# Optimization experiments

Hardware: AMD Instinct MI355X
Metric: run time of the kernel (lower is better)

Reference implementation:

```python
import jax, jax.numpy as jnp
import numpy as np
import math

EMBED_DIM = 2048
NUM_HEADS = 16
HEAD_DIM = EMBED_DIM // NUM_HEADS
SCALE = 1.0 / math.sqrt(HEAD_DIM)

# ALiBi slopes for power-of-2 num_heads: base = 2**(-2**(-(log2(H)-3))), slopes = base**i, i=1..H
_BASE = 2.0 ** (-2.0 ** (-(math.log2(NUM_HEADS) - 3)))
ALIBI_SLOPES = np.array([_BASE ** i for i in range(1, NUM_HEADS + 1)], dtype=np.float32)


def setup_inputs() -> dict:
    key = jax.random.key(0)
    ks = jax.random.split(key, 7)
    B, L, D, R_KV, R_Q = 2, 2048, EMBED_DIM, 512, 1536
    std = 0.02
    return {
        "hidden_states": jax.random.normal(ks[0], (B, L, D), jnp.float32),
        "Wq_down": jax.random.normal(ks[1], (R_Q, D), jnp.float32) * std,
        "Wq_up": jax.random.normal(ks[2], (NUM_HEADS * HEAD_DIM, R_Q), jnp.float32) * std,
        "Wkv_down": jax.random.normal(ks[3], (R_KV, D), jnp.float32) * std,
        "k_up": jax.random.normal(ks[4], (NUM_HEADS, R_KV, HEAD_DIM), jnp.float32) * std,
        "v_up": jax.random.normal(ks[5], (NUM_HEADS, R_KV, HEAD_DIM), jnp.float32) * std,
        "Wo": jax.random.normal(ks[6], (D, D), jnp.float32) * std,
    }


def reference(hidden_states, Wq_down, Wq_up, Wkv_down, k_up, v_up, Wo):
    B, L, D = hidden_states.shape
    # Query: low-rank down/up projection
    q = (hidden_states @ Wq_down.T) @ Wq_up.T            # [B, L, H*d]
    q = q.reshape(B, L, NUM_HEADS, HEAD_DIM).transpose(0, 2, 1, 3)  # [B, H, L, d]
    # Shared compressed latent KV
    c = hidden_states @ Wkv_down.T                        # [B, L, r]
    k = jnp.einsum('bsr,hrd->bhsd', c, k_up)              # [B, H, L, d]
    v = jnp.einsum('bsr,hrd->bhsd', c, v_up)
    scores = jnp.einsum('bhqd,bhkd->bhqk', q, k) * SCALE  # [B, H, L, L]
    # ALiBi bias: -slope_h * |i - j|
    pos = jnp.arange(L)
    dist = jnp.abs(pos[:, None] - pos[None, :]).astype(jnp.float32)
    slopes = jnp.asarray(ALIBI_SLOPES)
    scores = scores - slopes[None, :, None, None] * dist[None, None, :, :]
    # Causal mask
    causal = pos[:, None] >= pos[None, :]
    scores = jnp.where(causal[None, None], scores, -jnp.inf)
    attn = jax.nn.softmax(scores.astype(jnp.float32), axis=-1).astype(scores.dtype)
    out = jnp.einsum('bhqk,bhkd->bhqd', attn, v)          # [B, H, L, d]
    out = out.transpose(0, 2, 1, 3).reshape(B, L, D)
    return out @ Wo.T
```

## Files before the change

### kernel.cpp

```cpp
#include <hip/hip_runtime.h>
#include <math.h>

typedef __bf16 bf16;
typedef __bf16 bf16x8 __attribute__((ext_vector_type(8)));
typedef __bf16 bf16x4 __attribute__((ext_vector_type(4)));
typedef float f32x4 __attribute__((ext_vector_type(4)));

#define AS1 __attribute__((address_space(1)))
#define AS3 __attribute__((address_space(3)))

#define ATTN_BLOCKS 792
#define COMB_BLOCKS 168

struct ATables {
  int tbl[ATTN_BLOCKS * 2];
  int grp[COMB_BLOCKS * 4];
};

constexpr ATables make_tables() {
  ATables T{};
  int WH[16] = {22,32,45,64,90,128,181,256,362,512,724,1024,1448,2048,2896,4096};
  int nc = 0, np = 0, ng = 0;
  for (int qt = 15; qt >= 0; --qt)
    for (int h = 15; h >= 0; --h)
      for (int b = 0; b < 2; ++b) {
        int q0 = qt * 128, nkv = 2 * qt + 2;
        int dlo = q0 - WH[h];
        int kv_lo = dlo > 0 ? (dlo >> 6) : 0;
        int span = nkv - kv_lo;
        int nch = (span + 7) >> 3;
        int base = b | (h << 1) | (qt << 5);
        if (nch == 1) {
          T.tbl[2 * nc] = base | (kv_lo << 9) | (span << 16);
          T.tbl[2 * nc + 1] = -1;
          ++nc;
        } else {
          T.grp[4 * ng] = base; T.grp[4 * ng + 1] = np; T.grp[4 * ng + 2] = nch;
          ++ng;
          for (int c = 0; c < nch; ++c) {
            int cs = kv_lo + c * 8;
            int cl = nkv - cs; if (cl > 8) cl = 8;
            T.tbl[2 * nc] = base | (cs << 9) | (cl << 16);
            T.tbl[2 * nc + 1] = np;
            ++nc; ++np;
          }
        }
      }
  return T;
}

__device__ const ATables g_tab = make_tables();

__device__ __forceinline__ void g2l16(const void* g, void* l) {
  __builtin_amdgcn_global_load_lds((const AS1 void*)g, (AS3 void*)l, 16, 0, 0);
}

__device__ __forceinline__ void cvt_seg(const float* __restrict__ in,
                                        bf16* __restrict__ out, int n4) {
  int i = blockIdx.x * 256 + threadIdx.x;
  const int stride = gridDim.x * 256;
  for (; i < n4; i += stride) {
    float4 v = ((const float4*)in)[i];
    bf16x4 o;
    o[0] = (bf16)v.x; o[1] = (bf16)v.y; o[2] = (bf16)v.z; o[3] = (bf16)v.w;
    ((bf16x4*)out)[i] = o;
  }
}

__global__ __launch_bounds__(256) void cvt_f32_bf16(
    const float* __restrict__ in, bf16* __restrict__ out, int n4) {
  cvt_seg(in, out, n4);
}

__global__ __launch_bounds__(256) void cvt3_f32_bf16(
    const float* __restrict__ s0, bf16* __restrict__ d0, int n0,
    const float* __restrict__ s1, bf16* __restrict__ d1, int n1,
    const float* __restrict__ s2, bf16* __restrict__ d2, int n2) {
  cvt_seg(s0, d0, n0);
  cvt_seg(s1, d1, n1);
  cvt_seg(s2, d2, n2);
}

__global__ __launch_bounds__(256) void transpose_cvt(
    const float* __restrict__ in, bf16* __restrict__ out, int R, int D)
{
  __shared__ bf16 tile[64][72];
  const long long base = (long long)blockIdx.z * R * D;
  const int r0 = blockIdx.y * 64, c0 = blockIdx.x * 64;
  const int t = threadIdx.x;
#pragma unroll
  for (int i = 0; i < 4; ++i) {
    int c = i * 256 + t;
    int rr = c >> 4, cc = (c & 15) << 2;
    float4 v = *(const float4*)&in[base + (long long)(r0 + rr) * D + c0 + cc];
    tile[rr][cc + 0] = (bf16)v.x;
    tile[rr][cc + 1] = (bf16)v.y;
    tile[rr][cc + 2] = (bf16)v.z;
    tile[rr][cc + 3] = (bf16)v.w;
  }
  __syncthreads();
#pragma unroll
  for (int i = 0; i < 2; ++i) {
    int c = i * 256 + t;
    int rr = c >> 3, cc = (c & 7) << 3;
    bf16x8 v;
#pragma unroll
    for (int j = 0; j < 8; ++j) v[j] = tile[cc + j][rr];
    *(bf16x8*)&out[base + (long long)(c0 + rr) * R + r0 + cc] = v;
  }
}

template <typename CT>
__global__ __launch_bounds__(256) void gemm_nt(
    const bf16* __restrict__ A, const bf16* __restrict__ B, CT* __restrict__ C,
    int lda, int ldb, int ldc, int K, long long sA, long long sB, long long sC)
{
  A += (long long)blockIdx.z * sA;
  B += (long long)blockIdx.z * sB;
  C += (long long)blockIdx.z * sC;

  __shared__ bf16 As[128][64];
  __shared__ bf16 Bs[128][64];

  const int t = threadIdx.x;
  const int lane = t & 63, wave = t >> 6;
  const int wm = (wave >> 1) * 64, wn = (wave & 1) * 64;
  const int m0 = blockIdx.y * 128, n0 = blockIdx.x * 128;
  const int r16 = lane & 15, q8 = (lane >> 4) * 8;

  f32x4 acc[4][4] = {};

  for (int k0 = 0; k0 < K; k0 += 64) {
    __syncthreads();
#pragma unroll
    for (int r = 0; r < 4; ++r) {
      int c = r * 256 + t;
      int row = c >> 3, col = (c & 7) << 3;
      g2l16(A + (long long)(m0 + row) * lda + (k0 + col), &As[row][col]);
      g2l16(B + (long long)(n0 + row) * ldb + (k0 + col), &Bs[row][col]);
    }
    __syncthreads();

#pragma unroll
    for (int ks = 0; ks < 2; ++ks) {
      bf16x8 af[4], bfr[4];
#pragma unroll
      for (int i = 0; i < 4; ++i)
        af[i]  = *(const bf16x8*)&As[wm + i * 16 + r16][ks * 32 + q8];
#pragma unroll
      for (int i = 0; i < 4; ++i)
        bfr[i] = *(const bf16x8*)&Bs[wn + i * 16 + r16][ks * 32 + q8];
#pragma unroll
      for (int mi = 0; mi < 4; ++mi)
#pragma unroll
        for (int ni = 0; ni < 4; ++ni)
          acc[mi][ni] = __builtin_amdgcn_mfma_f32_16x16x32_bf16(af[mi], bfr[ni], acc[mi][ni], 0, 0, 0);
    }
  }

  const int quad = lane >> 4;
#pragma unroll
  for (int mi = 0; mi < 4; ++mi)
#pragma unroll
    for (int ni = 0; ni < 4; ++ni)
#pragma unroll
      for (int r = 0; r < 4; ++r) {
        int mm = m0 + wm + mi * 16 + quad * 4 + r;
        int nn = n0 + wn + ni * 16 + r16;
        C[(long long)mm * ldc + nn] = (CT)acc[mi][ni][r];
      }
}

__global__ __launch_bounds__(256) void gemm_qkv(
    const bf16* __restrict__ XCp, const bf16* __restrict__ Wqub,
    const bf16* __restrict__ kupT, const bf16* __restrict__ vupT,
    bf16* __restrict__ Qb, bf16* __restrict__ Kb, bf16* __restrict__ VTb)
{
  const bf16* Cl = XCp + 1536;
  const int g = blockIdx.x;
  const bf16 *A, *B;
  bf16* C;
  int lda, ldb, ldc, K, m0, n0;
  if (g < 512) {
    A = XCp; B = Wqub; C = Qb;
    lda = 2048; ldb = 1536; ldc = 2048; K = 1536;
    n0 = (g & 15) * 128; m0 = (g >> 4) * 128;
  } else if (g < 1024) {
    int i = g - 512, bz = i >> 5, by = i & 31;
    A = Cl; B = kupT + bz * 65536; C = Kb + (long long)bz * 524288;
    lda = 2048; ldb = 512; ldc = 128; K = 512;
    m0 = by * 128; n0 = 0;
  } else {
    int i = g - 1024, bz = i >> 5, bx = i & 31;
    A = vupT + bz * 65536; B = Cl; C = VTb + (long long)bz * 524288;
    lda = 512; ldb = 2048; ldc = 4096; K = 512;
    m0 = 0; n0 = bx * 128;
  }

  __shared__ bf16 As[128][64];
  __shared__ bf16 Bs[128][64];

  const int t = threadIdx.x;
  const int lane = t & 63, wave = t >> 6;
  const int wm = (wave >> 1) * 64, wn = (wave & 1) * 64;
  const int r16 = lane & 15, q8 = (lane >> 4) * 8;

  f32x4 acc[4][4] = {};

  for (int k0 = 0; k0 < K; k0 += 64) {
    __syncthreads();
#pragma unroll
    for (int r = 0; r < 4; ++r) {
      int c = r * 256 + t;
      int row = c >> 3, col = (c & 7) << 3;
      g2l16(A + (long long)(m0 + row) * lda + (k0 + col), &As[row][col]);
      g2l16(B + (long long)(n0 + row) * ldb + (k0 + col), &Bs[row][col]);
    }
    __syncthreads();

#pragma unroll
    for (int ks = 0; ks < 2; ++ks) {
      bf16x8 af[4], bfr[4];
#pragma unroll
      for (int i = 0; i < 4; ++i)
        af[i]  = *(const bf16x8*)&As[wm + i * 16 + r16][ks * 32 + q8];
#pragma unroll
      for (int i = 0; i < 4; ++i)
        bfr[i] = *(const bf16x8*)&Bs[wn + i * 16 + r16][ks * 32 + q8];
#pragma unroll
      for (int mi = 0; mi < 4; ++mi)
#pragma unroll
        for (int ni = 0; ni < 4; ++ni)
          acc[mi][ni] = __builtin_amdgcn_mfma_f32_16x16x32_bf16(af[mi], bfr[ni], acc[mi][ni], 0, 0, 0);
    }
  }

  const int quad = lane >> 4;
#pragma unroll
  for (int mi = 0; mi < 4; ++mi)
#pragma unroll
    for (int ni = 0; ni < 4; ++ni)
#pragma unroll
      for (int r = 0; r < 4; ++r) {
        int mm = m0 + wm + mi * 16 + quad * 4 + r;
        int nn = n0 + wn + ni * 16 + r16;
        C[(long long)mm * ldc + nn] = (bf16)acc[mi][ni][r];
      }
}

__global__ __launch_bounds__(256) void attn_kernel(
    const bf16* __restrict__ Q, const bf16* __restrict__ Kh,
    const bf16* __restrict__ VT, bf16* __restrict__ O,
    float* __restrict__ ml, bf16* __restrict__ parts)
{
  const int L = 2048, HD = 128, D = 2048;
  const int meta = g_tab.tbl[2 * blockIdx.x];
  const int part = g_tab.tbl[2 * blockIdx.x + 1];
  const int b = meta & 1, h = (meta >> 1) & 15, qt = (meta >> 5) & 15;
  const int cs = (meta >> 9) & 127, cl = (meta >> 16) & 15;
  const int q0 = qt * 128, nkv = 2 * qt + 2;
  const int cend = cs + cl;
  const int mraw = nkv - 2 > cs ? nkv - 2 : cs;
  const int mstart = mraw < cend ? mraw : cend;

  const int t = threadIdx.x, wave = t >> 6, lane = t & 63;
  const int col = lane & 15, quad = lane >> 4;
  const float LOG2E = 1.44269504f;
  const float slope2 = exp2f(-0.5f * (float)(h + 1)) * LOG2E;
  const float slope16 = slope2 * 16.0f;
  const float scale2 = 0.08838834764831845f * LOG2E;

  __shared__ bf16 Ksf[64 * 128];
  __shared__ bf16 Vsf[2][128 * 64];
  __shared__ bf16 Psf[128 * 64];

  const long long qrow0 = (long long)(b * L + q0 + wave * 32);
  const long long kbase = (long long)(h * 4096 + b * L) * HD;
  const long long vbase = (long long)(h * HD) * 4096 + b * L;

  auto stage = [&](int vbuf, int itile) {
    const int kv0 = itile << 6;
#pragma unroll
    for (int i = 0; i < 4; ++i) {
      int P = i * 256 + t;
      {
        int rr = P >> 4, cc = ((P & 15) ^ (rr & 15)) << 3;
        g2l16(Kh + kbase + (long long)(kv0 + rr) * HD + cc, &Ksf[P * 8]);
      }
      {
        int rr = P >> 3, cc = ((P & 7) ^ (rr & 7)) << 3;
        g2l16(VT + vbase + (long long)rr * 4096 + kv0 + cc, &Vsf[vbuf][P * 8]);
      }
    }
  };

  bf16x8 qf[2][4];
#pragma unroll
  for (int mi = 0; mi < 2; ++mi)
#pragma unroll
    for (int ks = 0; ks < 4; ++ks)
      qf[mi][ks] = *(const bf16x8*)&Q[(qrow0 + mi * 16 + col) * D + h * HD + ks * 32 + quad * 8];

  f32x4 o_acc[2][8] = {};
  float m_i[2][4], l_i[2][4];
#pragma unroll
  for (int mi = 0; mi < 2; ++mi)
#pragma unroll
    for (int r = 0; r < 4; ++r) { m_i[mi][r] = -1e30f; l_i[mi][r] = 0.f; }

  stage(0, cend - 1);

  for (int it = cend - 1; it >= cs; --it) {
    const int cur = (cend - 1 - it) & 1;
    const int kv0 = it << 6;
    const bool masked = (it >= mstart);

    __syncthreads();

    f32x4 s_acc[2][4] = {};
    __builtin_amdgcn_s_setprio(1);
#pragma unroll
    for (int ks = 0; ks < 4; ++ks) {
      bf16x8 kf[4];
#pragma unroll
      for (int ni = 0; ni < 4; ++ni)
        kf[ni] = *(const bf16x8*)&Ksf[(ni * 16 + col) * 128 +
                                      (((ks * 4 + quad) ^ col) << 3)];
#pragma unroll
      for (int mi = 0; mi < 2; ++mi)
#pragma unroll
        for (int ni = 0; ni < 4; ++ni)
          s_acc[mi][ni] = __builtin_amdgcn_mfma_f32_16x16x32_bf16(
              qf[mi][ks], kf[ni], s_acc[mi][ni], 0, 0, 0);
    }
    __builtin_amdgcn_s_setprio(0);

    __syncthreads();
    if (it > cs) stage(cur ^ 1, it - 1);

    float grow = -1e30f;
#pragma unroll
    for (int mi = 0; mi < 2; ++mi)
#pragma unroll
      for (int r = 0; r < 4; ++r) {
        const int rowq = wave * 32 + mi * 16 + quad * 4 + r;
        const int qg = q0 + rowq;
        const float sb = slope2 * (float)(qg - kv0 - col);
        float t0 = fmaxf(
            fmaxf(fmaf(s_acc[mi][0][r], scale2, 0.0f * slope16),
                  fmaf(s_acc[mi][1][r], scale2, 1.0f * slope16)),
            fmaxf(fmaf(s_acc[mi][2][r], scale2, 2.0f * slope16),
                  fmaf(s_acc[mi][3][r], scale2, 3.0f * slope16)));
        grow = fmaxf(grow, (t0 - sb) - m_i[mi][r]);
      }

    if (!__any(grow > 20.0f)) {
#pragma unroll
      for (int mi = 0; mi < 2; ++mi)
#pragma unroll
        for (int r = 0; r < 4; ++r) {
          const int rowq = wave * 32 + mi * 16 + quad * 4 + r;
          const int qg = q0 + rowq;
          const float c0 = -slope2 * (float)(qg - kv0 - col) - m_i[mi][r];
          float ps = 0.f;
#pragma unroll
          for (int ni = 0; ni < 4; ++ni) {
            float pv = exp2f(fmaf(s_acc[mi][ni][r], scale2,
                                  (float)ni * slope16 + c0));
            if (masked && (kv0 + ni * 16 + col > qg)) pv = 0.f;
            ps += pv;
            Psf[rowq * 64 + ((((ni * 2) + (col >> 3)) ^ (rowq & 7)) << 3) +
                (col & 7)] = (bf16)pv;
          }
          l_i[mi][r] += ps;
        }
    } else {
#pragma unroll
      for (int mi = 0; mi < 2; ++mi)
#pragma unroll
        for (int r = 0; r < 4; ++r) {
          const int rowq = wave * 32 + mi * 16 + quad * 4 + r;
          const int qg = q0 + rowq;
          const float sb = slope2 * (float)(qg - kv0 - col);
          float svv[4];
#pragma unroll
          for (int ni = 0; ni < 4; ++ni) {
            svv[ni] = fmaf(s_acc[mi][ni][r], scale2, (float)ni * slope16 - sb);
            if (masked && (kv0 + ni * 16 + col > qg)) svv[ni] = -1e30f;
          }
          float rm = fmaxf(fmaxf(svv[0], svv[1]), fmaxf(svv[2], svv[3]));
#pragma unroll
          for (int off = 1; off < 16; off <<= 1)
            rm = fmaxf(rm, __shfl_xor(rm, off, 64));
          const float mold = m_i[mi][r];
          float mnew = fmaxf(mold, rm);
          if (masked) mnew = fmaxf(mnew, -1e20f);
          const float alpha = exp2f(mold - mnew);
          float ps = 0.f;
#pragma unroll
          for (int ni = 0; ni < 4; ++ni) {
            float pv = exp2f(svv[ni] - mnew);
            ps += pv;
            Psf[rowq * 64 + ((((ni * 2) + (col >> 3)) ^ (rowq & 7)) << 3) +
                (col & 7)] = (bf16)pv;
          }
          l_i[mi][r] = fmaf(alpha, l_i[mi][r], ps);
          m_i[mi][r] = mnew;
#pragma unroll
          for (int di = 0; di < 8; ++di) o_acc[mi][di][r] *= alpha;
        }
    }

    __builtin_amdgcn_s_setprio(1);
#pragma unroll
    for (int kstep = 0; kstep < 2; ++kstep) {
      bf16x8 pf[2];
#pragma unroll
      for (int mi = 0; mi < 2; ++mi)
        pf[mi] = *(const bf16x8*)&Psf[(wave * 32 + mi * 16 + col) * 64 +
                                      (((kstep * 4 + quad) ^ (col & 7)) << 3)];
#pragma unroll
      for (int di = 0; di < 8; ++di) {
        bf16x8 vf = *(const bf16x8*)&Vsf[cur][(di * 16 + col) * 64 +
                                             (((kstep * 4 + quad) ^ (col & 7)) << 3)];
#pragma unroll
        for (int mi = 0; mi < 2; ++mi)
          o_acc[mi][di] = __builtin_amdgcn_mfma_f32_16x16x32_bf16(
              pf[mi], vf, o_acc[mi][di], 0, 0, 0);
      }
    }
    __builtin_amdgcn_s_setprio(0);
  }

  if (part < 0) {
#pragma unroll
    for (int mi = 0; mi < 2; ++mi)
#pragma unroll
      for (int r = 0; r < 4; ++r) {
        float lt = l_i[mi][r];
#pragma unroll
        for (int off = 1; off < 16; off <<= 1)
          lt += __shfl_xor(lt, off, 64);
        float rl = 1.0f / lt;
        long long qg = qrow0 + mi * 16 + quad * 4 + r;
#pragma unroll
        for (int di = 0; di < 8; ++di)
          O[qg * D + h * HD + di * 16 + col] = (bf16)(o_acc[mi][di][r] * rl);
      }
  } else {
    bf16* pb = parts + (long long)part * 16384;
    float* mlp = ml + (long long)part * 256;
#pragma unroll
    for (int mi = 0; mi < 2; ++mi)
#pragma unroll
      for (int r = 0; r < 4; ++r) {
        float lt = l_i[mi][r];
#pragma unroll
        for (int off = 1; off < 16; off <<= 1)
          lt += __shfl_xor(lt, off, 64);
        int rowq = wave * 32 + mi * 16 + quad * 4 + r;
        if (col == 0) { mlp[rowq] = m_i[mi][r]; mlp[128 + rowq] = lt; }
#pragma unroll
        for (int di = 0; di < 8; ++di)
          pb[rowq * 128 + di * 16 + col] = (bf16)o_acc[mi][di][r];
      }
  }
}

__global__ __launch_bounds__(256) void attn_combine(
    const float* __restrict__ ml, const bf16* __restrict__ parts,
    bf16* __restrict__ O)
{
  const int meta = g_tab.grp[4 * blockIdx.x];
  const int first = g_tab.grp[4 * blockIdx.x + 1];
  const int n = g_tab.grp[4 * blockIdx.x + 2];
  const int b = meta & 1, h = (meta >> 1) & 15, qt = (meta >> 5) & 15;
  const int t = threadIdx.x;
  const int row = t >> 1, cg = t & 1;

  float M = -1e30f;
  for (int c = 0; c < n; ++c) M = fmaxf(M, ml[(long long)(first + c) * 256 + row]);

  float acc[64];
#pragma unroll
  for (int j = 0; j < 64; ++j) acc[j] = 0.f;
  float den = 0.f;
  for (int c = 0; c < n; ++c) {
    const float* mlc = ml + (long long)(first + c) * 256;
    float w = exp2f(mlc[row] - M);
    den = fmaf(w, mlc[128 + row], den);
    const bf16* p = parts + (long long)(first + c) * 16384 + row * 128 + cg * 64;
#pragma unroll
    for (int j8 = 0; j8 < 8; ++j8) {
      bf16x8 v = ((const bf16x8*)p)[j8];
#pragma unroll
      for (int k = 0; k < 8; ++k) acc[j8 * 8 + k] = fmaf(w, (float)v[k], acc[j8 * 8 + k]);
    }
  }
  float rd = 1.0f / den;
  long long qg = (long long)b * 2048 + qt * 128 + row;
  bf16* o = O + qg * 2048 + h * 128 + cg * 64;
#pragma unroll
  for (int j8 = 0; j8 < 8; ++j8) {
    bf16x8 v;
#pragma unroll
    for (int k = 0; k < 8; ++k) v[k] = (bf16)(acc[j8 * 8 + k] * rd);
    ((bf16x8*)o)[j8] = v;
  }
}

extern "C" void kernel_launch(void* const* d_in, const int* in_sizes, int n_in,
                              void* d_out, int out_size, void* d_ws, size_t ws_size,
                              hipStream_t stream) {
  (void)in_sizes; (void)n_in; (void)out_size; (void)ws_size;
  const float* hs  = (const float*)d_in[0];
  const float* Wqd = (const float*)d_in[1];
  const float* Wqu = (const float*)d_in[2];
  const float* Wkv = (const float*)d_in[3];
  const float* kup = (const float*)d_in[4];
  const float* vup = (const float*)d_in[5];
  const float* Wo  = (const float*)d_in[6];
  float* out = (float*)d_out;

  char* ws = (char*)d_ws;
  bf16* hsb  = (bf16*)ws; ws += (size_t)4096 * 2048 * 2;
  bf16* Wdcb = (bf16*)ws; ws += (size_t)2048 * 2048 * 2;
  bf16* Wqub = (bf16*)ws; ws += (size_t)2048 * 1536 * 2;
  bf16* kupT = (bf16*)ws; ws += (size_t)16 * 128 * 512 * 2;
  bf16* vupT = (bf16*)ws; ws += (size_t)16 * 128 * 512 * 2;
  bf16* XC   = (bf16*)ws; ws += (size_t)4096 * 2048 * 2;
  bf16* Qb   = (bf16*)ws; ws += (size_t)4096 * 2048 * 2;
  bf16* Kb   = (bf16*)ws; ws += (size_t)16 * 4096 * 128 * 2;
  bf16* VTb  = (bf16*)ws; ws += (size_t)16 * 128 * 4096 * 2;
  bf16* Cl   = XC + 1536;
  bf16* Ob   = hsb;
  bf16* Wob  = XC;

  float* mld   = (float*)Wdcb;
  bf16*  parts = (bf16*)(mld + 448 * 256);

  cvt_f32_bf16<<<1024, 256, 0, stream>>>(hs, hsb, 4096 * 2048 / 4);
  cvt3_f32_bf16<<<1024, 256, 0, stream>>>(
      Wqd, Wdcb, 1536 * 2048 / 4,
      Wkv, Wdcb + (size_t)1536 * 2048, 512 * 2048 / 4,
      Wqu, Wqub, 2048 * 1536 / 4);
  transpose_cvt<<<dim3(2, 8, 16), 256, 0, stream>>>(kup, kupT, 512, 128);
  transpose_cvt<<<dim3(2, 8, 16), 256, 0, stream>>>(vup, vupT, 512, 128);

  gemm_nt<bf16><<<dim3(16, 32, 1), 256, 0, stream>>>(hsb, Wdcb, XC,
                                                     2048, 2048, 2048, 2048, 0, 0, 0);
  gemm_qkv<<<dim3(1536, 1, 1), 256, 0, stream>>>(XC, Wqub, kupT, vupT,
                                                 Qb, Kb, VTb);
  cvt_f32_bf16<<<512, 256, 0, stream>>>(Wo, Wob, 2048 * 2048 / 4);
  attn_kernel<<<dim3(ATTN_BLOCKS, 1, 1), 256, 0, stream>>>(Qb, Kb, VTb, Ob, mld, parts);
  attn_combine<<<dim3(COMB_BLOCKS, 1, 1), 256, 0, stream>>>(mld, parts, Ob);
  gemm_nt<float><<<dim3(16, 32, 1), 256, 0, stream>>>(Ob, Wob, out,
                                                      2048, 2048, 2048, 2048, 0, 0, 0);
}
```

Baseline: 392.6 us.

## Double-buffer LDS tiles in GEMM kernels to overlap global loads with MFMA

Both GEMM kernels move from a single shared-memory tile to two ping-pong buffers. The next K-slice is issued via g2l16 right after the barrier, while MFMAs run on the current buffer. The goal is to hide global-to-LDS latency behind compute and save one barrier per iteration. LDS use doubles to 64KB per block, which may lower occupancy. g2l16 is likely an async global-to-LDS load, and the single barrier has to order both the reads and the async writes correctly.

```diff
diff --git a/kernel.cpp b/kernel.cpp
--- a/kernel.cpp
+++ b/kernel.cpp
@@ -119,8 +119,8 @@
   B += (long long)blockIdx.z * sB;
   C += (long long)blockIdx.z * sC;
 
-  __shared__ bf16 As[128][64];
-  __shared__ bf16 Bs[128][64];
+  __shared__ bf16 As[2][128][64];
+  __shared__ bf16 Bs[2][128][64];
 
   const int t = threadIdx.x;
   const int lane = t & 63, wave = t >> 6;
@@ -128,28 +128,33 @@
   const int m0 = blockIdx.y * 128, n0 = blockIdx.x * 128;
   const int r16 = lane & 15, q8 = (lane >> 4) * 8;
 
-  f32x4 acc[4][4] = {};
-
-  for (int k0 = 0; k0 < K; k0 += 64) {
-    __syncthreads();
+  auto stage = [&](int buf, int k0) {
 #pragma unroll
     for (int r = 0; r < 4; ++r) {
       int c = r * 256 + t;
       int row = c >> 3, col = (c & 7) << 3;
-      g2l16(A + (long long)(m0 + row) * lda + (k0 + col), &As[row][col]);
-      g2l16(B + (long long)(n0 + row) * ldb + (k0 + col), &Bs[row][col]);
-    }
+      g2l16(A + (long long)(m0 + row) * lda + (k0 + col), &As[buf][row][col]);
+      g2l16(B + (long long)(n0 + row) * ldb + (k0 + col), &Bs[buf][row][col]);
+    }
+  };
+
+  f32x4 acc[4][4] = {};
+
+  stage(0, 0);
+  int cur = 0;
+  for (int k0 = 0; k0 < K; k0 += 64, cur ^= 1) {
     __syncthreads();
+    if (k0 + 64 < K) stage(cur ^ 1, k0 + 64);
 
 #pragma unroll
     for (int ks = 0; ks < 2; ++ks) {
       bf16x8 af[4], bfr[4];
 #pragma unroll
       for (int i = 0; i < 4; ++i)
-        af[i]  = *(const bf16x8*)&As[wm + i * 16 + r16][ks * 32 + q8];
+        af[i]  = *(const bf16x8*)&As[cur][wm + i * 16 + r16][ks * 32 + q8];
 #pragma unroll
       for (int i = 0; i < 4; ++i)
-        bfr[i] = *(const bf16x8*)&Bs[wn + i * 16 + r16][ks * 32 + q8];
+        bfr[i] = *(const bf16x8*)&Bs[cur][wn + i * 16 + r16][ks * 32 + q8];
 #pragma unroll
       for (int mi = 0; mi < 4; ++mi)
 #pragma unroll
@@ -197,36 +202,41 @@
     m0 = 0; n0 = bx * 128;
   }
 
-  __shared__ bf16 As[128][64];
-  __shared__ bf16 Bs[128][64];
+  __shared__ bf16 As[2][128][64];
+  __shared__ bf16 Bs[2][128][64];
 
   const int t = threadIdx.x;
   const int lane = t & 63, wave = t >> 6;
   const int wm = (wave >> 1) * 64, wn = (wave & 1) * 64;
   const int r16 = lane & 15, q8 = (lane >> 4) * 8;
 
-  f32x4 acc[4][4] = {};
-
-  for (int k0 = 0; k0 < K; k0 += 64) {
-    __syncthreads();
+  auto stage = [&](int buf, int k0) {
 #pragma unroll
     for (int r = 0; r < 4; ++r) {
       int c = r * 256 + t;
       int row = c >> 3, col = (c & 7) << 3;
-      g2l16(A + (long long)(m0 + row) * lda + (k0 + col), &As[row][col]);
-      g2l16(B + (long long)(n0 + row) * ldb + (k0 + col), &Bs[row][col]);
-    }
+      g2l16(A + (long long)(m0 + row) * lda + (k0 + col), &As[buf][row][col]);
+      g2l16(B + (long long)(n0 + row) * ldb + (k0 + col), &Bs[buf][row][col]);
+    }
+  };
+
+  f32x4 acc[4][4] = {};
+
+  stage(0, 0);
+  int cur = 0;
+  for (int k0 = 0; k0 < K; k0 += 64, cur ^= 1) {
     __syncthreads();
+    if (k0 + 64 < K) stage(cur ^ 1, k0 + 64);
 
 #pragma unroll
     for (int ks = 0; ks < 2; ++ks) {
       bf16x8 af[4], bfr[4];
 #pragma unroll
       for (int i = 0; i < 4; ++i)
-        af[i]  = *(const bf16x8*)&As[wm + i * 16 + r16][ks * 32 + q8];
+        af[i]  = *(const bf16x8*)&As[cur][wm + i * 16 + r16][ks * 32 + q8];
 #pragma unroll
       for (int i = 0; i < 4; ++i)
-        bfr[i] = *(const bf16x8*)&Bs[wn + i * 16 + r16][ks * 32 + q8];
+        bfr[i] = *(const bf16x8*)&Bs[cur][wn + i * 16 + r16][ks * 32 + q8];
 #pragma unroll
       for (int mi = 0; mi < 4; ++mi)
 #pragma unroll
```

After: 390.6 us. About the same (-0.5%).
